# Optimization experiments

Hardware: AMD Instinct MI355X
Metric: run time of the kernel (lower is better)

The kernel has to match this reference:

```python
import jax, jax.numpy as jnp
import numpy as np
from jax import lax

E = 300   # word embedding dim (hard-coded embedding_size in DMCNN)
P = 5     # position-feature dim
H = 200   # conv out channels
S = 256   # max_seq_len
L = 34    # num_labels
VOCAB = 21128


def setup_inputs() -> dict:
    key = jax.random.key(0)
    ks = jax.random.split(key, 7)
    B = 8
    return {
        "inputs": jax.random.randint(ks[0], (B, S), 0, VOCAB, dtype=jnp.int64),
        "word_emb": jax.random.normal(ks[1], (VOCAB, E), dtype=jnp.float32) * 0.02,
        "pf_emb": jax.random.normal(ks[2], (S, P), dtype=jnp.float32) * 0.02,
        "conv_W": jax.random.normal(ks[3], (H, E + P, 3), dtype=jnp.float32) * 0.02,
        "conv_b": jax.random.normal(ks[4], (H,), dtype=jnp.float32) * 0.02,
        "fc_W": jax.random.normal(ks[5], (L, 3 * E + 2 * H), dtype=jnp.float32) * 0.02,
        "fc_b": jax.random.normal(ks[6], (L,), dtype=jnp.float32) * 0.02,
    }


def _conv1d(x_ncs, w_oik):
    # x: [N, C, S], w: [O, I, K], stride 1, padding 1 (kernel 3)
    return lax.conv_general_dilated(
        x_ncs, w_oik, window_strides=(1,), padding=[(1, 1)],
        dimension_numbers=("NCH", "OIH", "NCH"))


def reference(inputs, word_emb, pf_emb, conv_W, conv_b, fc_W, fc_b):
    B = inputs.shape[0]
    tok = word_emb[inputs]                       # [B, S, E]

    # Positions i = 1 .. S-2 (the original loop), fully vectorized.
    i_vals = jnp.arange(1, S - 1)                # [S-2]
    j = jnp.arange(S)
    pos_idx = jnp.abs(j[None, :] - i_vals[:, None])   # [S-2, S] == the loop's pos_index
    pf = pf_emb[pos_idx]                         # [S-2, S, P]

    # Conv is linear: split into token part (shared across i) + pf part (per i).
    W_tok, W_pf = conv_W[:, :E, :], conv_W[:, E:, :]
    conv_tok = _conv1d(tok.transpose(0, 2, 1), W_tok) + conv_b[None, :, None]  # [B, H, S]
    conv_pf = _conv1d(pf.transpose(0, 2, 1), W_pf)                             # [S-2, H, S] (batch-independent)

    out = jax.nn.relu(conv_tok[None] + conv_pf[:, None])   # [S-2, B, H, S]

    # Dynamic split max-pool at index i.
    left_mask = (j[None, :] < i_vals[:, None])[:, None, None, :]  # [S-2,1,1,S]
    neg_inf = jnp.array(-jnp.inf, dtype=out.dtype)
    max_left = jnp.where(left_mask, out, neg_inf).max(axis=-1)    # [S-2, B, H]
    max_right = jnp.where(left_mask, neg_inf, out).max(axis=-1)   # [S-2, B, H]
    pool = jnp.concatenate([max_left, max_right], axis=-1)        # [S-2, B, 2H]

    # Lexical-level features: window [i-1, i, i+1] flattened.
    llf = jnp.concatenate([tok[:, 0:S - 2], tok[:, 1:S - 1], tok[:, 2:S]], axis=-1)  # [B, S-2, 3E]

    feat = jnp.concatenate([pool.transpose(1, 0, 2), llf], axis=-1)  # [B, S-2, 2H+3E]
    logits_mid = jnp.einsum("bsf,lf->bsl", feat, fc_W) + fc_b        # [B, S-2, L]

    pad = jnp.zeros((B, 1, L), dtype=logits_mid.dtype).at[:, :, -1].set(1.0)
    return jnp.concatenate([pad, logits_mid, pad], axis=1)          # [B, S, L]
```

## Files before the change

kernel.cpp:

```cpp
#include <hip/hip_runtime.h>

#define E 300
#define P 5
#define H 200
#define S 256
#define L 34
#define B 8
#define NI 254

typedef __attribute__((ext_vector_type(8))) _Float16 half8;
typedef __attribute__((ext_vector_type(2))) _Float16 h2;
typedef __attribute__((ext_vector_type(4))) float f32x4;

#define TOKB_OFF   0
#define WR3_OFF    309632
#define FCWB_OFF   406144
#define G_OFF      438400
#define C0_OFF     489600
#define C255_OFF   515000
#define CT_OFF     540400
#define POOLF_OFF  745200

__device__ __forceinline__ unsigned short f2h(float f) {
    _Float16 h = (_Float16)f;
    unsigned short u; __builtin_memcpy(&u, &h, 2);
    return u;
}
__device__ __forceinline__ h2 u2h2(unsigned u) {
    h2 h; __builtin_memcpy(&h, &u, 4); return h;
}
__device__ __forceinline__ unsigned h2u(h2 h) {
    unsigned u; __builtin_memcpy(&u, &h, 4); return u;
}
__device__ __forceinline__ h2 hmax2(h2 a, h2 b) {
    return __builtin_elementwise_max(a, b);
}
__device__ __forceinline__ half8 load_h8(const unsigned short* p) {
    half8 r;
    ((ushort4*)&r)[0] = *(const ushort4*)p;
    ((ushort4*)&r)[1] = *(const ushort4*)(p + 4);
    return r;
}

#define GA_BLOCKS   605
#define WR3_BLOCKS  754
#define FCW_BLOCKS  252
#define PREP_BLOCKS 64
#define INIT_BLOCKS (GA_BLOCKS + WR3_BLOCKS + FCW_BLOCKS + PREP_BLOCKS)

__global__ __launch_bounds__(256) void k_init(const int* __restrict__ ids,
                                              const float* __restrict__ we,
                                              const float* __restrict__ convW,
                                              const float* __restrict__ fcW,
                                              const float* __restrict__ pf,
                                              unsigned short* __restrict__ tokb,
                                              unsigned short* __restrict__ Wr3,
                                              unsigned short* __restrict__ fcWb,
                                              unsigned short* __restrict__ g,
                                              unsigned short* __restrict__ c0,
                                              unsigned short* __restrict__ c255) {
    int bx = blockIdx.x;
    if (bx < GA_BLOCKS) {
        int idx = bx * 256 + threadIdx.x;
        const int total = B * 258 * 75;
        if (idx >= total) return;
        int row = idx / 75;
        int col = idx - row * 75;
        int b = row / 258;
        int r = row - b * 258;
        float4 v = make_float4(0.f, 0.f, 0.f, 0.f);
        if (r >= 1 && r <= 256) {
            int id = ids[b * S + (r - 1)];
            v = ((const float4*)we)[(size_t)id * 75 + col];
        }
        ushort4 o;
        o.x = f2h(v.x); o.y = f2h(v.y); o.z = f2h(v.z); o.w = f2h(v.w);
        *(ushort4*)(tokb + (size_t)row * 300 + col * 4) = o;
        return;
    }
    if (bx < GA_BLOCKS + WR3_BLOCKS) {
        int idx = (bx - GA_BLOCKS) * 256 + threadIdx.x;
        if (idx < 193024) {
            int hh = idx / 928, kk = idx - hh * 928;
            float v = 0.f;
            if (hh < H && kk < 900) {
                int r = kk / 300, e = kk - r * 300;
                v = convW[hh * 915 + e * 3 + r];
            }
            Wr3[idx] = f2h(v);
        }
        return;
    }
    if (bx < GA_BLOCKS + WR3_BLOCKS + FCW_BLOCKS) {
        int t = (bx - GA_BLOCKS - WR3_BLOCKS) * 256 + threadIdx.x;
        if (t < 64512) {
            int l = t / 1344, c = t - l * 1344;
            float v = 0.f;
            if (l < L) {
                if (c < 400) v = fcW[l * 1300 + c];
                else if (c >= 416 && c < 1316) v = fcW[l * 1300 + 400 + (c - 416)];
            }
            fcWb[t] = f2h(v);
        }
        return;
    }
    {
        __shared__ float cwg[200 * 15];
        int tid = threadIdx.x;
        if (tid < 200) {
            const float* src = convW + tid * 915 + 900;
#pragma unroll
            for (int i = 0; i < 15; i++) cwg[tid * 15 + i] = src[i];
        }
        __syncthreads();
        if (tid >= 200) return;
        int h = tid;
        int pb = bx - (GA_BLOCKS + WR3_BLOCKS + FCW_BLOCKS);
#pragma unroll 1
        for (int rl = 0; rl < 16; rl++) {
            int rg = pb * 16 + rl;
            if (rg >= 1020) break;
            float a = 0.f;
            if (rg < 512) {
                int d = rg - 256;
#pragma unroll
                for (int k = 0; k < 3; k++) {
                    int r = d + k - 1; r = (r < 0) ? -r : r; if (r > 255) r = 255;
#pragma unroll
                    for (int q = 0; q < P; q++)
                        a += cwg[h * 15 + q * 3 + k] * pf[r * P + q];
                }
                g[rg * H + h] = f2h(a);
            } else if (rg < 766) {
                int m = rg - 512, i = m + 1;
#pragma unroll
                for (int q = 0; q < P; q++) {
                    a += cwg[h * 15 + q * 3 + 1] * pf[i * P + q];
                    a += cwg[h * 15 + q * 3 + 2] * pf[(i - 1) * P + q];
                }
                c0[m * H + h] = f2h(a);
            } else {
                int m = rg - 766, i = m + 1;
#pragma unroll
                for (int q = 0; q < P; q++) {
                    a += cwg[h * 15 + q * 3 + 0] * pf[(254 - i) * P + q];
                    a += cwg[h * 15 + q * 3 + 1] * pf[(255 - i) * P + q];
                }
                c255[m * H + h] = f2h(a);
            }
        }
    }
}

__global__ __launch_bounds__(512) void k_conv(const unsigned short* __restrict__ tokb,
                                              const unsigned short* __restrict__ Wr3,
                                              const float* __restrict__ convB,
                                              unsigned short* __restrict__ ct) {
    __shared__ float4 cld[4 * 64];
    int n0 = blockIdx.x * 16;
    int mg = blockIdx.y;
    int tid = threadIdx.x;
    int wave = tid >> 6;
    int lane = tid & 63;
    int mt = wave & 3;
    int kh = wave >> 2;
    int quad = lane >> 4;
    int lr = lane & 15;
    int mtile = mg * 4 + mt;
    int b = mtile >> 4;
    int j0 = (mtile & 15) << 4;

    const unsigned short* pa = tokb + ((size_t)(b * 258 + j0 + lr) * 300 + quad * 8);
    const unsigned short* pb = Wr3 + ((size_t)(n0 + lr) * 928 + quad * 8);

    f32x4 acc0 = {0.f, 0.f, 0.f, 0.f};
    f32x4 acc1 = {0.f, 0.f, 0.f, 0.f};
    if (kh == 0) {
#pragma unroll
        for (int kk = 0; kk < 14; kk += 2) {
            half8 a0 = load_h8(pa + kk * 32);
            half8 b0 = load_h8(pb + kk * 32);
            acc0 = __builtin_amdgcn_mfma_f32_16x16x32_f16(a0, b0, acc0, 0, 0, 0);
            half8 a1 = load_h8(pa + kk * 32 + 32);
            half8 b1 = load_h8(pb + kk * 32 + 32);
            acc1 = __builtin_amdgcn_mfma_f32_16x16x32_f16(a1, b1, acc1, 0, 0, 0);
        }
    } else {
#pragma unroll
        for (int kk = 14; kk + 1 < 29; kk += 2) {
            half8 a0 = load_h8(pa + kk * 32);
            half8 b0 = load_h8(pb + kk * 32);
            acc0 = __builtin_amdgcn_mfma_f32_16x16x32_f16(a0, b0, acc0, 0, 0, 0);
            half8 a1 = load_h8(pa + kk * 32 + 32);
            half8 b1 = load_h8(pb + kk * 32 + 32);
            acc1 = __builtin_amdgcn_mfma_f32_16x16x32_f16(a1, b1, acc1, 0, 0, 0);
        }
        {
            half8 a0 = load_h8(pa + 28 * 32);
            half8 b0 = load_h8(pb + 28 * 32);
            acc0 = __builtin_amdgcn_mfma_f32_16x16x32_f16(a0, b0, acc0, 0, 0, 0);
        }
    }
    f32x4 accw = acc0 + acc1;
    if (kh == 1) {
        cld[mt * 64 + lane] = make_float4(accw[0], accw[1], accw[2], accw[3]);
    }
    __syncthreads();
    if (kh == 0) {
        float4 p = cld[mt * 64 + lane];
        int h = n0 + lr;
        if (h < H) {
            float bias = convB[h];
            ct[(size_t)(b * 256 + j0 + quad * 4 + 0) * 200 + h] = f2h(accw[0] + p.x + bias);
            ct[(size_t)(b * 256 + j0 + quad * 4 + 1) * 200 + h] = f2h(accw[1] + p.y + bias);
            ct[(size_t)(b * 256 + j0 + quad * 4 + 2) * 200 + h] = f2h(accw[2] + p.z + bias);
            ct[(size_t)(b * 256 + j0 + quad * 4 + 3) * 200 + h] = f2h(accw[3] + p.w + bias);
        }
    }
}

__global__ __launch_bounds__(512) void k_poolA(const unsigned short* __restrict__ ct,
                                               const unsigned short* __restrict__ g,
                                               const unsigned short* __restrict__ c0,
                                               const unsigned short* __restrict__ c255,
                                               unsigned short* __restrict__ poolf) {
    __shared__ uint2 lds2[8 * 4 * 2 * 50];
    int pg = blockIdx.x;
    int b  = blockIdx.y;
    int tid = threadIdx.x;
    int sub = tid >> 6;
    int lane = tid & 63;
    int p0 = pg * 4 + 1;

    if (lane < 50) {
        int h = lane << 2;
        const unsigned short* ctb = ct + (size_t)b * S * H + h;
        const unsigned short* gb  = g + h;

        h2 z = {(_Float16)0, (_Float16)0};
        h2 aL0a=z, aL0b=z, aL1a=z, aL1b=z, aL2a=z, aL2b=z, aL3a=z, aL3b=z;
        h2 aR0a=z, aR0b=z, aR1a=z, aR1b=z, aR2a=z, aR2b=z, aR3a=z, aR3b=z;

        if (sub == 0) {
            uint2 cu = *(const uint2*)ctb;
            h2 ca = u2h2(cu.x), cb = u2h2(cu.y);
            int m = pg * 4;
            if (m + 0 < NI) { uint2 t = *(const uint2*)(c0 + (m+0) * H + h);
                aL0a = hmax2(aL0a, ca + u2h2(t.x)); aL0b = hmax2(aL0b, cb + u2h2(t.y)); }
            if (m + 1 < NI) { uint2 t = *(const uint2*)(c0 + (m+1) * H + h);
                aL1a = hmax2(aL1a, ca + u2h2(t.x)); aL1b = hmax2(aL1b, cb + u2h2(t.y)); }
            if (m + 2 < NI) { uint2 t = *(const uint2*)(c0 + (m+2) * H + h);
                aL2a = hmax2(aL2a, ca + u2h2(t.x)); aL2b = hmax2(aL2b, cb + u2h2(t.y)); }
            if (m + 3 < NI) { uint2 t = *(const uint2*)(c0 + (m+3) * H + h);
                aL3a = hmax2(aL3a, ca + u2h2(t.x)); aL3b = hmax2(aL3b, cb + u2h2(t.y)); }
        }
        if (sub == 7) {
            uint2 cu = *(const uint2*)(ctb + (size_t)255 * H);
            h2 ca = u2h2(cu.x), cb = u2h2(cu.y);
            int m = pg * 4;
            if (m + 0 < NI) { uint2 t = *(const uint2*)(c255 + (m+0) * H + h);
                aR0a = hmax2(aR0a, ca + u2h2(t.x)); aR0b = hmax2(aR0b, cb + u2h2(t.y)); }
            if (m + 1 < NI) { uint2 t = *(const uint2*)(c255 + (m+1) * H + h);
                aR1a = hmax2(aR1a, ca + u2h2(t.x)); aR1b = hmax2(aR1b, cb + u2h2(t.y)); }
            if (m + 2 < NI) { uint2 t = *(const uint2*)(c255 + (m+2) * H + h);
                aR2a = hmax2(aR2a, ca + u2h2(t.x)); aR2b = hmax2(aR2b, cb + u2h2(t.y)); }
            if (m + 3 < NI) { uint2 t = *(const uint2*)(c255 + (m+3) * H + h);
                aR3a = hmax2(aR3a, ca + u2h2(t.x)); aR3b = hmax2(aR3b, cb + u2h2(t.y)); }
        }

        int js = (sub == 0) ? 1 : sub * 32;
        int je = (sub == 7) ? 254 : sub * 32 + 31;

        uint2 gu;
        gu = *(const uint2*)(gb + (size_t)(js - p0 + 256) * H); h2 gr0a = u2h2(gu.x), gr0b = u2h2(gu.y);
        gu = *(const uint2*)(gb + (size_t)(js - p0 + 255) * H); h2 gr1a = u2h2(gu.x), gr1b = u2h2(gu.y);
        gu = *(const uint2*)(gb + (size_t)(js - p0 + 254) * H); h2 gr2a = u2h2(gu.x), gr2b = u2h2(gu.y);
        gu = *(const uint2*)(gb + (size_t)(js - p0 + 253) * H); h2 gr3a = u2h2(gu.x), gr3b = u2h2(gu.y);

        int eL = (je + 1 < p0) ? (je + 1) : p0;
        int mS = (js > p0) ? js : p0;
        int eM = (je + 1 < p0 + 4) ? (je + 1) : (p0 + 4);
        int rS = (js > p0 + 4) ? js : (p0 + 4);

#pragma unroll 4
        for (int j = js; j < eL; ++j) {
            uint2 cu = *(const uint2*)(ctb + (size_t)j * H);
            h2 ca = u2h2(cu.x), cb = u2h2(cu.y);
            aL0a = hmax2(aL0a, ca + gr0a); aL0b = hmax2(aL0b, cb + gr0b);
            aL1a = hmax2(aL1a, ca + gr1a); aL1b = hmax2(aL1b, cb + gr1b);
            aL2a = hmax2(aL2a, ca + gr2a); aL2b = hmax2(aL2b, cb + gr2b);
            aL3a = hmax2(aL3a, ca + gr3a); aL3b = hmax2(aL3b, cb + gr3b);
            gr3a = gr2a; gr3b = gr2b; gr2a = gr1a; gr2b = gr1b; gr1a = gr0a; gr1b = gr0b;
            uint2 gn = *(const uint2*)(gb + (size_t)(j + 1 - p0 + 256) * H);
            gr0a = u2h2(gn.x); gr0b = u2h2(gn.y);
        }
        for (int j = mS; j < eM; ++j) {
            uint2 cu = *(const uint2*)(ctb + (size_t)j * H);
            h2 ca = u2h2(cu.x), cb = u2h2(cu.y);
            h2 v0a = ca + gr0a, v0b = cb + gr0b;
            h2 v1a = ca + gr1a, v1b = cb + gr1b;
            h2 v2a = ca + gr2a, v2b = cb + gr2b;
            h2 v3a = ca + gr3a, v3b = cb + gr3b;
            if (j < p0)     { aL0a = hmax2(aL0a, v0a); aL0b = hmax2(aL0b, v0b); }
            else            { aR0a = hmax2(aR0a, v0a); aR0b = hmax2(aR0b, v0b); }
            if (j < p0 + 1) { aL1a = hmax2(aL1a, v1a); aL1b = hmax2(aL1b, v1b); }
            else            { aR1a = hmax2(aR1a, v1a); aR1b = hmax2(aR1b, v1b); }
            if (j < p0 + 2) { aL2a = hmax2(aL2a, v2a); aL2b = hmax2(aL2b, v2b); }
            else            { aR2a = hmax2(aR2a, v2a); aR2b = hmax2(aR2b, v2b); }
            if (j < p0 + 3) { aL3a = hmax2(aL3a, v3a); aL3b = hmax2(aL3b, v3b); }
            else            { aR3a = hmax2(aR3a, v3a); aR3b = hmax2(aR3b, v3b); }
            gr3a = gr2a; gr3b = gr2b; gr2a = gr1a; gr2b = gr1b; gr1a = gr0a; gr1b = gr0b;
            uint2 gn = *(const uint2*)(gb + (size_t)(j + 1 - p0 + 256) * H);
            gr0a = u2h2(gn.x); gr0b = u2h2(gn.y);
        }
#pragma unroll 4
        for (int j = rS; j <= je; ++j) {
            uint2 cu = *(const uint2*)(ctb + (size_t)j * H);
            h2 ca = u2h2(cu.x), cb = u2h2(cu.y);
            aR0a = hmax2(aR0a, ca + gr0a); aR0b = hmax2(aR0b, cb + gr0b);
            aR1a = hmax2(aR1a, ca + gr1a); aR1b = hmax2(aR1b, cb + gr1b);
            aR2a = hmax2(aR2a, ca + gr2a); aR2b = hmax2(aR2b, cb + gr2b);
            aR3a = hmax2(aR3a, ca + gr3a); aR3b = hmax2(aR3b, cb + gr3b);
            gr3a = gr2a; gr3b = gr2b; gr2a = gr1a; gr2b = gr1b; gr1a = gr0a; gr1b = gr0b;
            uint2 gn = *(const uint2*)(gb + (size_t)(j + 1 - p0 + 256) * H);
            gr0a = u2h2(gn.x); gr0b = u2h2(gn.y);
        }

        uint2* lp = lds2 + (size_t)sub * 400 + lane;
        lp[0]   = make_uint2(h2u(aL0a), h2u(aL0b)); lp[50]  = make_uint2(h2u(aR0a), h2u(aR0b));
        lp[100] = make_uint2(h2u(aL1a), h2u(aL1b)); lp[150] = make_uint2(h2u(aR1a), h2u(aR1b));
        lp[200] = make_uint2(h2u(aL2a), h2u(aL2b)); lp[250] = make_uint2(h2u(aR2a), h2u(aR2b));
        lp[300] = make_uint2(h2u(aL3a), h2u(aL3b)); lp[350] = make_uint2(h2u(aR3a), h2u(aR3b));
    }
    __syncthreads();

    if (tid < 400) {
        int k = tid / 100;
        int r = tid - k * 100;
        int hf = r / 50;
        int ln = r - hf * 50;
        int slot = (k * 2 + hf) * 50 + ln;
        uint2 v = lds2[slot];
        h2 va = u2h2(v.x), vb = u2h2(v.y);
#pragma unroll
        for (int s2 = 1; s2 < 8; s2++) {
            uint2 w = lds2[s2 * 400 + slot];
            va = hmax2(va, u2h2(w.x));
            vb = hmax2(vb, u2h2(w.y));
        }
        int m = pg * 4 + k;
        if (m < NI)
            *(uint2*)(poolf + (size_t)(b * 256 + m + 1) * 416 + hf * 200 + ln * 4)
                = make_uint2(h2u(va), h2u(vb));
    } else if (tid < 464) {
        int t = tid - 400;
        int k = t >> 4, c = t & 15;
        int m = pg * 4 + k;
        if (m < NI) poolf[(size_t)(b * 256 + m + 1) * 416 + 400 + c] = 0;
    }
}

__global__ __launch_bounds__(512) void k_fc(const unsigned short* __restrict__ poolf,
                                            const unsigned short* __restrict__ tokb,
                                            const unsigned short* __restrict__ fcWb,
                                            const float* __restrict__ fcB,
                                            float* __restrict__ out) {
    __shared__ float4 cld[3 * 2 * 64];
    int n0 = blockIdx.x * 16;
    int mg = blockIdx.y;
    int tid = threadIdx.x;
    int wave = tid >> 6;
    int lane = tid & 63;
    int mt = wave & 1;
    int kp = wave >> 1;
    int quad = lane >> 4;
    int lr = lane & 15;
    int mtile = mg * 2 + mt;
    int b = mtile >> 4;
    int s0 = (mtile & 15) << 4;

    const unsigned short* pa0 = poolf + ((size_t)(b * 256 + s0 + lr) * 416 + quad * 8);
    const unsigned short* pb0 = fcWb + ((size_t)(n0 + lr) * 1344 + quad * 8);
    const unsigned short* pa1 = tokb + ((size_t)(b * 258 + s0 + lr) * 300 + quad * 8);
    const unsigned short* pb1 = fcWb + ((size_t)(n0 + lr) * 1344 + 416 + quad * 8);

    f32x4 acc0 = {0.f, 0.f, 0.f, 0.f};
    f32x4 acc1 = {0.f, 0.f, 0.f, 0.f};
    if (kp == 0) {
#pragma unroll
        for (int u = 0; u + 1 < 11; u += 2) {
            half8 a0 = load_h8(pa0 + u * 32);
            half8 b0 = load_h8(pb0 + u * 32);
            acc0 = __builtin_amdgcn_mfma_f32_16x16x32_f16(a0, b0, acc0, 0, 0, 0);
            half8 a1 = load_h8(pa0 + u * 32 + 32);
            half8 b1 = load_h8(pb0 + u * 32 + 32);
            acc1 = __builtin_amdgcn_mfma_f32_16x16x32_f16(a1, b1, acc1, 0, 0, 0);
        }
        {
            half8 a0 = load_h8(pa0 + 10 * 32);
            half8 b0 = load_h8(pb0 + 10 * 32);
            acc0 = __builtin_amdgcn_mfma_f32_16x16x32_f16(a0, b0, acc0, 0, 0, 0);
        }
    } else if (kp == 1) {
        {
            half8 a0 = load_h8(pa0 + 11 * 32);
            half8 b0 = load_h8(pb0 + 11 * 32);
            acc0 = __builtin_amdgcn_mfma_f32_16x16x32_f16(a0, b0, acc0, 0, 0, 0);
            half8 a1 = load_h8(pa0 + 12 * 32);
            half8 b1 = load_h8(pb0 + 12 * 32);
            acc1 = __builtin_amdgcn_mfma_f32_16x16x32_f16(a1, b1, acc1, 0, 0, 0);
        }
#pragma unroll
        for (int v = 0; v + 1 < 9; v += 2) {
            half8 a0 = load_h8(pa1 + v * 32);
            half8 b0 = load_h8(pb1 + v * 32);
            acc0 = __builtin_amdgcn_mfma_f32_16x16x32_f16(a0, b0, acc0, 0, 0, 0);
            half8 a1 = load_h8(pa1 + v * 32 + 32);
            half8 b1 = load_h8(pb1 + v * 32 + 32);
            acc1 = __builtin_amdgcn_mfma_f32_16x16x32_f16(a1, b1, acc1, 0, 0, 0);
        }
        {
            half8 a0 = load_h8(pa1 + 8 * 32);
            half8 b0 = load_h8(pb1 + 8 * 32);
            acc0 = __builtin_amdgcn_mfma_f32_16x16x32_f16(a0, b0, acc0, 0, 0, 0);
        }
    } else if (kp == 2) {
#pragma unroll
        for (int v = 9; v + 1 < 19; v += 2) {
            half8 a0 = load_h8(pa1 + v * 32);
            half8 b0 = load_h8(pb1 + v * 32);
            acc0 = __builtin_amdgcn_mfma_f32_16x16x32_f16(a0, b0, acc0, 0, 0, 0);
            half8 a1 = load_h8(pa1 + v * 32 + 32);
            half8 b1 = load_h8(pb1 + v * 32 + 32);
            acc1 = __builtin_amdgcn_mfma_f32_16x16x32_f16(a1, b1, acc1, 0, 0, 0);
        }
    } else {
#pragma unroll
        for (int v = 19; v + 1 < 29; v += 2) {
            half8 a0 = load_h8(pa1 + v * 32);
            half8 b0 = load_h8(pb1 + v * 32);
            acc0 = __builtin_amdgcn_mfma_f32_16x16x32_f16(a0, b0, acc0, 0, 0, 0);
            half8 a1 = load_h8(pa1 + v * 32 + 32);
            half8 b1 = load_h8(pb1 + v * 32 + 32);
            acc1 = __builtin_amdgcn_mfma_f32_16x16x32_f16(a1, b1, acc1, 0, 0, 0);
        }
    }
    f32x4 accw = acc0 + acc1;
    if (kp > 0) {
        cld[((kp - 1) * 2 + mt) * 64 + lane] = make_float4(accw[0], accw[1], accw[2], accw[3]);
    }
    __syncthreads();
    if (kp == 0) {
        float4 p1 = cld[(0 * 2 + mt) * 64 + lane];
        float4 p2 = cld[(1 * 2 + mt) * 64 + lane];
        float4 p3 = cld[(2 * 2 + mt) * 64 + lane];
        float r4[4] = {accw[0] + p1.x + p2.x + p3.x,
                       accw[1] + p1.y + p2.y + p3.y,
                       accw[2] + p1.z + p2.z + p3.z,
                       accw[3] + p1.w + p2.w + p3.w};
        int l = n0 + lr;
        if (l < L) {
            float bias = fcB[l];
#pragma unroll
            for (int r = 0; r < 4; r++) {
                int s = s0 + quad * 4 + r;
                float val;
                if (s == 0 || s == S - 1) val = (l == L - 1) ? 1.0f : 0.0f;
                else                      val = r4[r] + bias;
                out[(size_t)(b * 256 + s) * L + l] = val;
            }
        }
    }
}

extern "C" void kernel_launch(void* const* d_in, const int* in_sizes, int n_in,
                              void* d_out, int out_size, void* d_ws, size_t ws_size,
                              hipStream_t stream) {
    const int*   ids      = (const int*)d_in[0];
    const float* word_emb = (const float*)d_in[1];
    const float* pf_emb   = (const float*)d_in[2];
    const float* conv_W   = (const float*)d_in[3];
    const float* conv_b   = (const float*)d_in[4];
    const float* fc_W     = (const float*)d_in[5];
    const float* fc_b     = (const float*)d_in[6];
    float* out = (float*)d_out;
    float* ws  = (float*)d_ws;

    unsigned short* tokb  = (unsigned short*)(ws + TOKB_OFF);
    unsigned short* Wr3   = (unsigned short*)(ws + WR3_OFF);
    unsigned short* fcWb  = (unsigned short*)(ws + FCWB_OFF);
    unsigned short* g     = (unsigned short*)(ws + G_OFF);
    unsigned short* c0    = (unsigned short*)(ws + C0_OFF);
    unsigned short* c255  = (unsigned short*)(ws + C255_OFF);
    unsigned short* ct    = (unsigned short*)(ws + CT_OFF);
    unsigned short* poolf = (unsigned short*)(ws + POOLF_OFF);

    k_init<<<INIT_BLOCKS, 256, 0, stream>>>(ids, word_emb, conv_W, fc_W,
                                            pf_emb, tokb, Wr3, fcWb,
                                            g, c0, c255);
    k_conv<<<dim3(13, 32), 512, 0, stream>>>(tokb, Wr3, conv_b, ct);
    k_poolA<<<dim3(64, 8), 512, 0, stream>>>(ct, g, c0, c255, poolf);
    k_fc<<<dim3(3, 64), 512, 0, stream>>>(poolf, tokb, fcWb, fc_b, out);
}
```

Measured before the change: 114.5 us.

## Fuse conv, pool and fc kernels into one persistent kernel with grid barriers

Merges the three dependent kernels (conv GEMM, split max-pool, fc GEMM) into a single 512-block launch. A hierarchical atomic grid barrier in workspace memory separates the stages, and a memset clears it before each run. This removes two kernel launch boundaries and their drain and ramp gaps. In exchange it adds a memset launch and atomic spin-waits, and it relies on all 512 blocks being co-resident; the spin has a timeout break that could silently yield wrong results if they are not.

```diff
diff --git a/kernel.cpp b/kernel.cpp
--- a/kernel.cpp
+++ b/kernel.cpp
@@ -7,6 +7,8 @@
 #define L 34
 #define B 8
 #define NI 254
+#define NBLK 512
+#define NGRP 8
 
 typedef __attribute__((ext_vector_type(8))) _Float16 half8;
 typedef __attribute__((ext_vector_type(2))) _Float16 h2;
@@ -20,6 +22,7 @@
 #define C255_OFF   515000
 #define CT_OFF     540400
 #define POOLF_OFF  745200
+#define BAR_OFF    2000000
 
 __device__ __forceinline__ unsigned short f2h(float f) {
     _Float16 h = (_Float16)f;
@@ -47,6 +50,27 @@
 #define FCW_BLOCKS  252
 #define PREP_BLOCKS 64
 #define INIT_BLOCKS (GA_BLOCKS + WR3_BLOCKS + FCW_BLOCKS + PREP_BLOCKS)
+
+__device__ __forceinline__ void gbar(unsigned* bar, int phase) {
+    __syncthreads();
+    if (threadIdx.x == 0) {
+        unsigned* base = bar + phase * 1024;
+        unsigned* c1 = base + (blockIdx.x >> 6) * 16;
+        unsigned* c2 = base + 1008;
+        unsigned prev = __hip_atomic_fetch_add(c1, 1u, __ATOMIC_ACQ_REL,
+                                               __HIP_MEMORY_SCOPE_AGENT);
+        if (prev == 63)
+            __hip_atomic_fetch_add(c2, 1u, __ATOMIC_ACQ_REL,
+                                   __HIP_MEMORY_SCOPE_AGENT);
+        unsigned t = 0;
+        while (__hip_atomic_load(c2, __ATOMIC_ACQUIRE,
+                                 __HIP_MEMORY_SCOPE_AGENT) < NGRP) {
+            __builtin_amdgcn_s_sleep(2);
+            if (++t > (1u << 22)) break;
+        }
+    }
+    __syncthreads();
+}
 
 __global__ __launch_bounds__(256) void k_init(const int* __restrict__ ids,
                                               const float* __restrict__ we,
@@ -152,322 +176,328 @@
     }
 }
 
-__global__ __launch_bounds__(512) void k_conv(const unsigned short* __restrict__ tokb,
-                                              const unsigned short* __restrict__ Wr3,
-                                              const float* __restrict__ convB,
-                                              unsigned short* __restrict__ ct) {
-    __shared__ float4 cld[4 * 64];
-    int n0 = blockIdx.x * 16;
-    int mg = blockIdx.y;
-    int tid = threadIdx.x;
-    int wave = tid >> 6;
-    int lane = tid & 63;
-    int mt = wave & 3;
-    int kh = wave >> 2;
-    int quad = lane >> 4;
-    int lr = lane & 15;
-    int mtile = mg * 4 + mt;
-    int b = mtile >> 4;
-    int j0 = (mtile & 15) << 4;
-
-    const unsigned short* pa = tokb + ((size_t)(b * 258 + j0 + lr) * 300 + quad * 8);
-    const unsigned short* pb = Wr3 + ((size_t)(n0 + lr) * 928 + quad * 8);
-
-    f32x4 acc0 = {0.f, 0.f, 0.f, 0.f};
-    f32x4 acc1 = {0.f, 0.f, 0.f, 0.f};
-    if (kh == 0) {
-#pragma unroll
-        for (int kk = 0; kk < 14; kk += 2) {
-            half8 a0 = load_h8(pa + kk * 32);
-            half8 b0 = load_h8(pb + kk * 32);
-            acc0 = __builtin_amdgcn_mfma_f32_16x16x32_f16(a0, b0, acc0, 0, 0, 0);
-            half8 a1 = load_h8(pa + kk * 32 + 32);
-            half8 b1 = load_h8(pb + kk * 32 + 32);
-            acc1 = __builtin_amdgcn_mfma_f32_16x16x32_f16(a1, b1, acc1, 0, 0, 0);
-        }
-    } else {
-#pragma unroll
-        for (int kk = 14; kk + 1 < 29; kk += 2) {
-            half8 a0 = load_h8(pa + kk * 32);
-            half8 b0 = load_h8(pb + kk * 32);
-            acc0 = __builtin_amdgcn_mfma_f32_16x16x32_f16(a0, b0, acc0, 0, 0, 0);
-            half8 a1 = load_h8(pa + kk * 32 + 32);
-            half8 b1 = load_h8(pb + kk * 32 + 32);
-            acc1 = __builtin_amdgcn_mfma_f32_16x16x32_f16(a1, b1, acc1, 0, 0, 0);
-        }
-        {
-            half8 a0 = load_h8(pa + 28 * 32);
-            half8 b0 = load_h8(pb + 28 * 32);
-            acc0 = __builtin_amdgcn_mfma_f32_16x16x32_f16(a0, b0, acc0, 0, 0, 0);
-        }
-    }
-    f32x4 accw = acc0 + acc1;
-    if (kh == 1) {
-        cld[mt * 64 + lane] = make_float4(accw[0], accw[1], accw[2], accw[3]);
-    }
-    __syncthreads();
-    if (kh == 0) {
-        float4 p = cld[mt * 64 + lane];
-        int h = n0 + lr;
-        if (h < H) {
-            float bias = convB[h];
-            ct[(size_t)(b * 256 + j0 + quad * 4 + 0) * 200 + h] = f2h(accw[0] + p.x + bias);
-            ct[(size_t)(b * 256 + j0 + quad * 4 + 1) * 200 + h] = f2h(accw[1] + p.y + bias);
-            ct[(size_t)(b * 256 + j0 + quad * 4 + 2) * 200 + h] = f2h(accw[2] + p.z + bias);
-            ct[(size_t)(b * 256 + j0 + quad * 4 + 3) * 200 + h] = f2h(accw[3] + p.w + bias);
-        }
-    }
-}
-
-__global__ __launch_bounds__(512) void k_poolA(const unsigned short* __restrict__ ct,
-                                               const unsigned short* __restrict__ g,
-                                               const unsigned short* __restrict__ c0,
-                                               const unsigned short* __restrict__ c255,
-                                               unsigned short* __restrict__ poolf) {
-    __shared__ uint2 lds2[8 * 4 * 2 * 50];
-    int pg = blockIdx.x;
-    int b  = blockIdx.y;
-    int tid = threadIdx.x;
-    int sub = tid >> 6;
-    int lane = tid & 63;
-    int p0 = pg * 4 + 1;
-
-    if (lane < 50) {
-        int h = lane << 2;
-        const unsigned short* ctb = ct + (size_t)b * S * H + h;
-        const unsigned short* gb  = g + h;
-
-        h2 z = {(_Float16)0, (_Float16)0};
-        h2 aL0a=z, aL0b=z, aL1a=z, aL1b=z, aL2a=z, aL2b=z, aL3a=z, aL3b=z;
-        h2 aR0a=z, aR0b=z, aR1a=z, aR1b=z, aR2a=z, aR2b=z, aR3a=z, aR3b=z;
-
-        if (sub == 0) {
-            uint2 cu = *(const uint2*)ctb;
-            h2 ca = u2h2(cu.x), cb = u2h2(cu.y);
-            int m = pg * 4;
-            if (m + 0 < NI) { uint2 t = *(const uint2*)(c0 + (m+0) * H + h);
-                aL0a = hmax2(aL0a, ca + u2h2(t.x)); aL0b = hmax2(aL0b, cb + u2h2(t.y)); }
-            if (m + 1 < NI) { uint2 t = *(const uint2*)(c0 + (m+1) * H + h);
-                aL1a = hmax2(aL1a, ca + u2h2(t.x)); aL1b = hmax2(aL1b, cb + u2h2(t.y)); }
-            if (m + 2 < NI) { uint2 t = *(const uint2*)(c0 + (m+2) * H + h);
-                aL2a = hmax2(aL2a, ca + u2h2(t.x)); aL2b = hmax2(aL2b, cb + u2h2(t.y)); }
-            if (m + 3 < NI) { uint2 t = *(const uint2*)(c0 + (m+3) * H + h);
-                aL3a = hmax2(aL3a, ca + u2h2(t.x)); aL3b = hmax2(aL3b, cb + u2h2(t.y)); }
-        }
-        if (sub == 7) {
-            uint2 cu = *(const uint2*)(ctb + (size_t)255 * H);
-            h2 ca = u2h2(cu.x), cb = u2h2(cu.y);
-            int m = pg * 4;
-            if (m + 0 < NI) { uint2 t = *(const uint2*)(c255 + (m+0) * H + h);
-                aR0a = hmax2(aR0a, ca + u2h2(t.x)); aR0b = hmax2(aR0b, cb + u2h2(t.y)); }
-            if (m + 1 < NI) { uint2 t = *(const uint2*)(c255 + (m+1) * H + h);
-                aR1a = hmax2(aR1a, ca + u2h2(t.x)); aR1b = hmax2(aR1b, cb + u2h2(t.y)); }
-            if (m + 2 < NI) { uint2 t = *(const uint2*)(c255 + (m+2) * H + h);
-                aR2a = hmax2(aR2a, ca + u2h2(t.x)); aR2b = hmax2(aR2b, cb + u2h2(t.y)); }
-            if (m + 3 < NI) { uint2 t = *(const uint2*)(c255 + (m+3) * H + h);
-                aR3a = hmax2(aR3a, ca + u2h2(t.x)); aR3b = hmax2(aR3b, cb + u2h2(t.y)); }
-        }
-
-        int js = (sub == 0) ? 1 : sub * 32;
-        int je = (sub == 7) ? 254 : sub * 32 + 31;
-
-        uint2 gu;
-        gu = *(const uint2*)(gb + (size_t)(js - p0 + 256) * H); h2 gr0a = u2h2(gu.x), gr0b = u2h2(gu.y);
-        gu = *(const uint2*)(gb + (size_t)(js - p0 + 255) * H); h2 gr1a = u2h2(gu.x), gr1b = u2h2(gu.y);
-        gu = *(const uint2*)(gb + (size_t)(js - p0 + 254) * H); h2 gr2a = u2h2(gu.x), gr2b = u2h2(gu.y);
-        gu = *(const uint2*)(gb + (size_t)(js - p0 + 253) * H); h2 gr3a = u2h2(gu.x), gr3b = u2h2(gu.y);
-
-        int eL = (je + 1 < p0) ? (je + 1) : p0;
-        int mS = (js > p0) ? js : p0;
-        int eM = (je + 1 < p0 + 4) ? (je + 1) : (p0 + 4);
-        int rS = (js > p0 + 4) ? js : (p0 + 4);
+__global__ __launch_bounds__(512, 4) void k_bcd(
+        const unsigned short* __restrict__ tokb,
+        const unsigned short* __restrict__ Wr3,
+        const float* __restrict__ convB,
+        const unsigned short* __restrict__ g,
+        const unsigned short* __restrict__ c0,
+        const unsigned short* __restrict__ c255,
+        const unsigned short* __restrict__ fcWb,
+        const float* __restrict__ fcB,
+        unsigned short* __restrict__ ct,
+        unsigned short* __restrict__ poolf,
+        float* __restrict__ out,
+        unsigned* bar) {
+    __shared__ __align__(16) unsigned char smem[25600];
+    float4* cld = (float4*)smem;
+    uint2*  lds2 = (uint2*)smem;
+
+    const int bid = blockIdx.x;
+    const int tid = threadIdx.x;
+
+    if (bid < 416) {
+        int n0 = (bid % 13) * 16;
+        int mg = bid / 13;
+        int wave = tid >> 6;
+        int lane = tid & 63;
+        int mt = wave & 3;
+        int kh = wave >> 2;
+        int quad = lane >> 4;
+        int lr = lane & 15;
+        int mtile = mg * 4 + mt;
+        int b = mtile >> 4;
+        int j0 = (mtile & 15) << 4;
+
+        const unsigned short* pa = tokb + ((size_t)(b * 258 + j0 + lr) * 300 + quad * 8);
+        const unsigned short* pb = Wr3 + ((size_t)(n0 + lr) * 928 + quad * 8);
+
+        f32x4 acc0 = {0.f, 0.f, 0.f, 0.f};
+        f32x4 acc1 = {0.f, 0.f, 0.f, 0.f};
+        if (kh == 0) {
+#pragma unroll
+            for (int kk = 0; kk < 14; kk += 2) {
+                half8 a0 = load_h8(pa + kk * 32);
+                half8 b0 = load_h8(pb + kk * 32);
+                acc0 = __builtin_amdgcn_mfma_f32_16x16x32_f16(a0, b0, acc0, 0, 0, 0);
+                half8 a1 = load_h8(pa + kk * 32 + 32);
+                half8 b1 = load_h8(pb + kk * 32 + 32);
+                acc1 = __builtin_amdgcn_mfma_f32_16x16x32_f16(a1, b1, acc1, 0, 0, 0);
+            }
+        } else {
+#pragma unroll
+            for (int kk = 14; kk + 1 < 29; kk += 2) {
+                half8 a0 = load_h8(pa + kk * 32);
+                half8 b0 = load_h8(pb + kk * 32);
+                acc0 = __builtin_amdgcn_mfma_f32_16x16x32_f16(a0, b0, acc0, 0, 0, 0);
+                half8 a1 = load_h8(pa + kk * 32 + 32);
+                half8 b1 = load_h8(pb + kk * 32 + 32);
+                acc1 = __builtin_amdgcn_mfma_f32_16x16x32_f16(a1, b1, acc1, 0, 0, 0);
+            }
+            {
+                half8 a0 = load_h8(pa + 28 * 32);
+                half8 b0 = load_h8(pb + 28 * 32);
+                acc0 = __builtin_amdgcn_mfma_f32_16x16x32_f16(a0, b0, acc0, 0, 0, 0);
+            }
+        }
+        f32x4 accw = acc0 + acc1;
+        if (kh == 1) {
+            cld[mt * 64 + lane] = make_float4(accw[0], accw[1], accw[2], accw[3]);
+        }
+        __syncthreads();
+        if (kh == 0) {
+            float4 p = cld[mt * 64 + lane];
+            int h = n0 + lr;
+            if (h < H) {
+                float bias = convB[h];
+                ct[(size_t)(b * 256 + j0 + quad * 4 + 0) * 200 + h] = f2h(accw[0] + p.x + bias);
+                ct[(size_t)(b * 256 + j0 + quad * 4 + 1) * 200 + h] = f2h(accw[1] + p.y + bias);
+                ct[(size_t)(b * 256 + j0 + quad * 4 + 2) * 200 + h] = f2h(accw[2] + p.z + bias);
+                ct[(size_t)(b * 256 + j0 + quad * 4 + 3) * 200 + h] = f2h(accw[3] + p.w + bias);
+            }
+        }
+    }
+    gbar(bar, 0);
+
+    {
+        int pg = bid & 63;
+        int b  = bid >> 6;
+        int sub = tid >> 6;
+        int lane = tid & 63;
+        int p0 = pg * 4 + 1;
+
+        if (lane < 50) {
+            int h = lane << 2;
+            const unsigned short* ctb = ct + (size_t)b * S * H + h;
+            const unsigned short* gb  = g + h;
+
+            h2 z = {(_Float16)0, (_Float16)0};
+            h2 aL0a=z, aL0b=z, aL1a=z, aL1b=z, aL2a=z, aL2b=z, aL3a=z, aL3b=z;
+            h2 aR0a=z, aR0b=z, aR1a=z, aR1b=z, aR2a=z, aR2b=z, aR3a=z, aR3b=z;
+
+            if (sub == 0) {
+                uint2 cu = *(const uint2*)ctb;
+                h2 ca = u2h2(cu.x), cb = u2h2(cu.y);
+                int m = pg * 4;
+                if (m + 0 < NI) { uint2 t = *(const uint2*)(c0 + (m+0) * H + h);
+                    aL0a = hmax2(aL0a, ca + u2h2(t.x)); aL0b = hmax2(aL0b, cb + u2h2(t.y)); }
+                if (m + 1 < NI) { uint2 t = *(const uint2*)(c0 + (m+1) * H + h);
+                    aL1a = hmax2(aL1a, ca + u2h2(t.x)); aL1b = hmax2(aL1b, cb + u2h2(t.y)); }
+                if (m + 2 < NI) { uint2 t = *(const uint2*)(c0 + (m+2) * H + h);
+                    aL2a = hmax2(aL2a, ca + u2h2(t.x)); aL2b = hmax2(aL2b, cb + u2h2(t.y)); }
+                if (m + 3 < NI) { uint2 t = *(const uint2*)(c0 + (m+3) * H + h);
+                    aL3a = hmax2(aL3a, ca + u2h2(t.x)); aL3b = hmax2(aL3b, cb + u2h2(t.y)); }
+            }
+            if (sub == 7) {
+                uint2 cu = *(const uint2*)(ctb + (size_t)255 * H);
+                h2 ca = u2h2(cu.x), cb = u2h2(cu.y);
+                int m = pg * 4;
+                if (m + 0 < NI) { uint2 t = *(const uint2*)(c255 + (m+0) * H + h);
+                    aR0a = hmax2(aR0a, ca + u2h2(t.x)); aR0b = hmax2(aR0b, cb + u2h2(t.y)); }
+                if (m + 1 < NI) { uint2 t = *(const uint2*)(c255 + (m+1) * H + h);
+                    aR1a = hmax2(aR1a, ca + u2h2(t.x)); aR1b = hmax2(aR1b, cb + u2h2(t.y)); }
+                if (m + 2 < NI) { uint2 t = *(const uint2*)(c255 + (m+2) * H + h);
+                    aR2a = hmax2(aR2a, ca + u2h2(t.x)); aR2b = hmax2(aR2b, cb + u2h2(t.y)); }
+                if (m + 3 < NI) { uint2 t = *(const uint2*)(c255 + (m+3) * H + h);
+                    aR3a = hmax2(aR3a, ca + u2h2(t.x)); aR3b = hmax2(aR3b, cb + u2h2(t.y)); }
+            }
+
+            int js = (sub == 0) ? 1 : sub * 32;
+            int je = (sub == 7) ? 254 : sub * 32 + 31;
+
+            uint2 gu;
+            gu = *(const uint2*)(gb + (size_t)(js - p0 + 256) * H); h2 gr0a = u2h2(gu.x), gr0b = u2h2(gu.y);
+            gu = *(const uint2*)(gb + (size_t)(js - p0 + 255) * H); h2 gr1a = u2h2(gu.x), gr1b = u2h2(gu.y);
+            gu = *(const uint2*)(gb + (size_t)(js - p0 + 254) * H); h2 gr2a = u2h2(gu.x), gr2b = u2h2(gu.y);
+            gu = *(const uint2*)(gb + (size_t)(js - p0 + 253) * H); h2 gr3a = u2h2(gu.x), gr3b = u2h2(gu.y);
+
+            int eL = (je + 1 < p0) ? (je + 1) : p0;
+            int mS = (js > p0) ? js : p0;
+            int eM = (je + 1 < p0 + 4) ? (je + 1) : (p0 + 4);
+            int rS = (js > p0 + 4) ? js : (p0 + 4);
 
 #pragma unroll 4
-        for (int j = js; j < eL; ++j) {
-            uint2 cu = *(const uint2*)(ctb + (size_t)j * H);
-            h2 ca = u2h2(cu.x), cb = u2h2(cu.y);
-            aL0a = hmax2(aL0a, ca + gr0a); aL0b = hmax2(aL0b, cb + gr0b);
-            aL1a = hmax2(aL1a, ca + gr1a); aL1b = hmax2(aL1b, cb + gr1b);
-            aL2a = hmax2(aL2a, ca + gr2a); aL2b = hmax2(aL2b, cb + gr2b);
-            aL3a = hmax2(aL3a, ca + gr3a); aL3b = hmax2(aL3b, cb + gr3b);
-            gr3a = gr2a; gr3b = gr2b; gr2a = gr1a; gr2b = gr1b; gr1a = gr0a; gr1b = gr0b;
-            uint2 gn = *(const uint2*)(gb + (size_t)(j + 1 - p0 + 256) * H);
-            gr0a = u2h2(gn.x); gr0b = u2h2(gn.y);
-        }
-        for (int j = mS; j < eM; ++j) {
-            uint2 cu = *(const uint2*)(ctb + (size_t)j * H);
-            h2 ca = u2h2(cu.x), cb = u2h2(cu.y);
-            h2 v0a = ca + gr0a, v0b = cb + gr0b;
-            h2 v1a = ca + gr1a, v1b = cb + gr1b;
-            h2 v2a = ca + gr2a, v2b = cb + gr2b;
-            h2 v3a = ca + gr3a, v3b = cb + gr3b;
-            if (j < p0)     { aL0a = hmax2(aL0a, v0a); aL0b = hmax2(aL0b, v0b); }
-            else            { aR0a = hmax2(aR0a, v0a); aR0b = hmax2(aR0b, v0b); }
-            if (j < p0 + 1) { aL1a = hmax2(aL1a, v1a); aL1b = hmax2(aL1b, v1b); }
-            else            { aR1a = hmax2(aR1a, v1a); aR1b = hmax2(aR1b, v1b); }
-            if (j < p0 + 2) { aL2a = hmax2(aL2a, v2a); aL2b = hmax2(aL2b, v2b); }
-            else            { aR2a = hmax2(aR2a, v2a); aR2b = hmax2(aR2b, v2b); }
-            if (j < p0 + 3) { aL3a = hmax2(aL3a, v3a); aL3b = hmax2(aL3b, v3b); }
-            else            { aR3a = hmax2(aR3a, v3a); aR3b = hmax2(aR3b, v3b); }
-            gr3a = gr2a; gr3b = gr2b; gr2a = gr1a; gr2b = gr1b; gr1a = gr0a; gr1b = gr0b;
-            uint2 gn = *(const uint2*)(gb + (size_t)(j + 1 - p0 + 256) * H);
-            gr0a = u2h2(gn.x); gr0b = u2h2(gn.y);
-        }
+            for (int j = js; j < eL; ++j) {
+                uint2 cu = *(const uint2*)(ctb + (size_t)j * H);
+                h2 ca = u2h2(cu.x), cb = u2h2(cu.y);
+                aL0a = hmax2(aL0a, ca + gr0a); aL0b = hmax2(aL0b, cb + gr0b);
+                aL1a = hmax2(aL1a, ca + gr1a); aL1b = hmax2(aL1b, cb + gr1b);
+                aL2a = hmax2(aL2a, ca + gr2a); aL2b = hmax2(aL2b, cb + gr2b);
+                aL3a = hmax2(aL3a, ca + gr3a); aL3b = hmax2(aL3b, cb + gr3b);
+                gr3a = gr2a; gr3b = gr2b; gr2a = gr1a; gr2b = gr1b; gr1a = gr0a; gr1b = gr0b;
+                uint2 gn = *(const uint2*)(gb + (size_t)(j + 1 - p0 + 256) * H);
+                gr0a = u2h2(gn.x); gr0b = u2h2(gn.y);
+            }
+            for (int j = mS; j < eM; ++j) {
+                uint2 cu = *(const uint2*)(ctb + (size_t)j * H);
+                h2 ca = u2h2(cu.x), cb = u2h2(cu.y);
+                h2 v0a = ca + gr0a, v0b = cb + gr0b;
+                h2 v1a = ca + gr1a, v1b = cb + gr1b;
+                h2 v2a = ca + gr2a, v2b = cb + gr2b;
+                h2 v3a = ca + gr3a, v3b = cb + gr3b;
+                if (j < p0)     { aL0a = hmax2(aL0a, v0a); aL0b = hmax2(aL0b, v0b); }
+                else            { aR0a = hmax2(aR0a, v0a); aR0b = hmax2(aR0b, v0b); }
+                if (j < p0 + 1) { aL1a = hmax2(aL1a, v1a); aL1b = hmax2(aL1b, v1b); }
+                else            { aR1a = hmax2(aR1a, v1a); aR1b = hmax2(aR1b, v1b); }
+                if (j < p0 + 2) { aL2a = hmax2(aL2a, v2a); aL2b = hmax2(aL2b, v2b); }
+                else            { aR2a = hmax2(aR2a, v2a); aR2b = hmax2(aR2b, v2b); }
+                if (j < p0 + 3) { aL3a = hmax2(aL3a, v3a); aL3b = hmax2(aL3b, v3b); }
+                else            { aR3a = hmax2(aR3a, v3a); aR3b = hmax2(aR3b, v3b); }
+                gr3a = gr2a; gr3b = gr2b; gr2a = gr1a; gr2b = gr1b; gr1a = gr0a; gr1b = gr0b;
+                uint2 gn = *(const uint2*)(gb + (size_t)(j + 1 - p0 + 256) * H);
+                gr0a = u2h2(gn.x); gr0b = u2h2(gn.y);
+            }
 #pragma unroll 4
-        for (int j = rS; j <= je; ++j) {
-            uint2 cu = *(const uint2*)(ctb + (size_t)j * H);
-            h2 ca = u2h2(cu.x), cb = u2h2(cu.y);
-            aR0a = hmax2(aR0a, ca + gr0a); aR0b = hmax2(aR0b, cb + gr0b);
-            aR1a = hmax2(aR1a, ca + gr1a); aR1b = hmax2(aR1b, cb + gr1b);
-            aR2a = hmax2(aR2a, ca + gr2a); aR2b = hmax2(aR2b, cb + gr2b);
-            aR3a = hmax2(aR3a, ca + gr3a); aR3b = hmax2(aR3b, cb + gr3b);
-            gr3a = gr2a; gr3b = gr2b; gr2a = gr1a; gr2b = gr1b; gr1a = gr0a; gr1b = gr0b;
-            uint2 gn = *(const uint2*)(gb + (size_t)(j + 1 - p0 + 256) * H);
-            gr0a = u2h2(gn.x); gr0b = u2h2(gn.y);
-        }
-
-        uint2* lp = lds2 + (size_t)sub * 400 + lane;
-        lp[0]   = make_uint2(h2u(aL0a), h2u(aL0b)); lp[50]  = make_uint2(h2u(aR0a), h2u(aR0b));
-        lp[100] = make_uint2(h2u(aL1a), h2u(aL1b)); lp[150] = make_uint2(h2u(aR1a), h2u(aR1b));
-        lp[200] = make_uint2(h2u(aL2a), h2u(aL2b)); lp[250] = make_uint2(h2u(aR2a), h2u(aR2b));
-        lp[300] = make_uint2(h2u(aL3a), h2u(aL3b)); lp[350] = make_uint2(h2u(aR3a), h2u(aR3b));
-    }
-    __syncthreads();
-
-    if (tid < 400) {
-        int k = tid / 100;
-        int r = tid - k * 100;
-        int hf = r / 50;
-        int ln = r - hf * 50;
-        int slot = (k * 2 + hf) * 50 + ln;
-        uint2 v = lds2[slot];
-        h2 va = u2h2(v.x), vb = u2h2(v.y);
-#pragma unroll
-        for (int s2 = 1; s2 < 8; s2++) {
-            uint2 w = lds2[s2 * 400 + slot];
-            va = hmax2(va, u2h2(w.x));
-            vb = hmax2(vb, u2h2(w.y));
-        }
-        int m = pg * 4 + k;
-        if (m < NI)
-            *(uint2*)(poolf + (size_t)(b * 256 + m + 1) * 416 + hf * 200 + ln * 4)
-                = make_uint2(h2u(va), h2u(vb));
-    } else if (tid < 464) {
-        int t = tid - 400;
-        int k = t >> 4, c = t & 15;
-        int m = pg * 4 + k;
-        if (m < NI) poolf[(size_t)(b * 256 + m + 1) * 416 + 400 + c] = 0;
-    }
-}
-
-__global__ __launch_bounds__(512) void k_fc(const unsigned short* __restrict__ poolf,
-                                            const unsigned short* __restrict__ tokb,
-                                            const unsigned short* __restrict__ fcWb,
-                                            const float* __restrict__ fcB,
-                                            float* __restrict__ out) {
-    __shared__ float4 cld[3 * 2 * 64];
-    int n0 = blockIdx.x * 16;
-    int mg = blockIdx.y;
-    int tid = threadIdx.x;
-    int wave = tid >> 6;
-    int lane = tid & 63;
-    int mt = wave & 1;
-    int kp = wave >> 1;
-    int quad = lane >> 4;
-    int lr = lane & 15;
-    int mtile = mg * 2 + mt;
-    int b = mtile >> 4;
-    int s0 = (mtile & 15) << 4;
-
-    const unsigned short* pa0 = poolf + ((size_t)(b * 256 + s0 + lr) * 416 + quad * 8);
-    const unsigned short* pb0 = fcWb + ((size_t)(n0 + lr) * 1344 + quad * 8);
-    const unsigned short* pa1 = tokb + ((size_t)(b * 258 + s0 + lr) * 300 + quad * 8);
-    const unsigned short* pb1 = fcWb + ((size_t)(n0 + lr) * 1344 + 416 + quad * 8);
-
-    f32x4 acc0 = {0.f, 0.f, 0.f, 0.f};
-    f32x4 acc1 = {0.f, 0.f, 0.f, 0.f};
-    if (kp == 0) {
-#pragma unroll
-        for (int u = 0; u + 1 < 11; u += 2) {
-            half8 a0 = load_h8(pa0 + u * 32);
-            half8 b0 = load_h8(pb0 + u * 32);
-            acc0 = __builtin_amdgcn_mfma_f32_16x16x32_f16(a0, b0, acc0, 0, 0, 0);
-            half8 a1 = load_h8(pa0 + u * 32 + 32);
-            half8 b1 = load_h8(pb0 + u * 32 + 32);
-            acc1 = __builtin_amdgcn_mfma_f32_16x16x32_f16(a1, b1, acc1, 0, 0, 0);
-        }
-        {
-            half8 a0 = load_h8(pa0 + 10 * 32);
-            half8 b0 = load_h8(pb0 + 10 * 32);
-            acc0 = __builtin_amdgcn_mfma_f32_16x16x32_f16(a0, b0, acc0, 0, 0, 0);
-        }
-    } else if (kp == 1) {
-        {
-            half8 a0 = load_h8(pa0 + 11 * 32);
-            half8 b0 = load_h8(pb0 + 11 * 32);
-            acc0 = __builtin_amdgcn_mfma_f32_16x16x32_f16(a0, b0, acc0, 0, 0, 0);
-            half8 a1 = load_h8(pa0 + 12 * 32);
-            half8 b1 = load_h8(pb0 + 12 * 32);
-            acc1 = __builtin_amdgcn_mfma_f32_16x16x32_f16(a1, b1, acc1, 0, 0, 0);
-        }
-#pragma unroll
-        for (int v = 0; v + 1 < 9; v += 2) {
-            half8 a0 = load_h8(pa1 + v * 32);
-            half8 b0 = load_h8(pb1 + v * 32);
-            acc0 = __builtin_amdgcn_mfma_f32_16x16x32_f16(a0, b0, acc0, 0, 0, 0);
-            half8 a1 = load_h8(pa1 + v * 32 + 32);
-            half8 b1 = load_h8(pb1 + v * 32 + 32);
-            acc1 = __builtin_amdgcn_mfma_f32_16x16x32_f16(a1, b1, acc1, 0, 0, 0);
-        }
-        {
-            half8 a0 = load_h8(pa1 + 8 * 32);
-            half8 b0 = load_h8(pb1 + 8 * 32);
-            acc0 = __builtin_amdgcn_mfma_f32_16x16x32_f16(a0, b0, acc0, 0, 0, 0);
-        }
-    } else if (kp == 2) {
-#pragma unroll
-        for (int v = 9; v + 1 < 19; v += 2) {
-            half8 a0 = load_h8(pa1 + v * 32);
-            half8 b0 = load_h8(pb1 + v * 32);
-            acc0 = __builtin_amdgcn_mfma_f32_16x16x32_f16(a0, b0, acc0, 0, 0, 0);
-            half8 a1 = load_h8(pa1 + v * 32 + 32);
-            half8 b1 = load_h8(pb1 + v * 32 + 32);
-            acc1 = __builtin_amdgcn_mfma_f32_16x16x32_f16(a1, b1, acc1, 0, 0, 0);
-        }
-    } else {
-#pragma unroll
-        for (int v = 19; v + 1 < 29; v += 2) {
-            half8 a0 = load_h8(pa1 + v * 32);
-            half8 b0 = load_h8(pb1 + v * 32);
-            acc0 = __builtin_amdgcn_mfma_f32_16x16x32_f16(a0, b0, acc0, 0, 0, 0);
-            half8 a1 = load_h8(pa1 + v * 32 + 32);
-            half8 b1 = load_h8(pb1 + v * 32 + 32);
-            acc1 = __builtin_amdgcn_mfma_f32_16x16x32_f16(a1, b1, acc1, 0, 0, 0);
-        }
-    }
-    f32x4 accw = acc0 + acc1;
-    if (kp > 0) {
-        cld[((kp - 1) * 2 + mt) * 64 + lane] = make_float4(accw[0], accw[1], accw[2], accw[3]);
-    }
-    __syncthreads();
-    if (kp == 0) {
-        float4 p1 = cld[(0 * 2 + mt) * 64 + lane];
-        float4 p2 = cld[(1 * 2 + mt) * 64 + lane];
-        float4 p3 = cld[(2 * 2 + mt) * 64 + lane];
-        float r4[4] = {accw[0] + p1.x + p2.x + p3.x,
-                       accw[1] + p1.y + p2.y + p3.y,
-                       accw[2] + p1.z + p2.z + p3.z,
-                       accw[3] + p1.w + p2.w + p3.w};
-        int l = n0 + lr;
-        if (l < L) {
-            float bias = fcB[l];
-#pragma unroll
-            for (int r = 0; r < 4; r++) {
-                int s = s0 + quad * 4 + r;
-                float val;
-                if (s == 0 || s == S - 1) val = (l == L - 1) ? 1.0f : 0.0f;
-                else                      val = r4[r] + bias;
-                out[(size_t)(b * 256 + s) * L + l] = val;
+            for (int j = rS; j <= je; ++j) {
+                uint2 cu = *(const uint2*)(ctb + (size_t)j * H);
+                h2 ca = u2h2(cu.x), cb = u2h2(cu.y);
+                aR0a = hmax2(aR0a, ca + gr0a); aR0b = hmax2(aR0b, cb + gr0b);
+                aR1a = hmax2(aR1a, ca + gr1a); aR1b = hmax2(aR1b, cb + gr1b);
+                aR2a = hmax2(aR2a, ca + gr2a); aR2b = hmax2(aR2b, cb + gr2b);
+                aR3a = hmax2(aR3a, ca + gr3a); aR3b = hmax2(aR3b, cb + gr3b);
+                gr3a = gr2a; gr3b = gr2b; gr2a = gr1a; gr2b = gr1b; gr1a = gr0a; gr1b = gr0b;
+                uint2 gn = *(const uint2*)(gb + (size_t)(j + 1 - p0 + 256) * H);
+                gr0a = u2h2(gn.x); gr0b = u2h2(gn.y);
+            }
+
+            uint2* lp = lds2 + (size_t)sub * 400 + lane;
+            lp[0]   = make_uint2(h2u(aL0a), h2u(aL0b)); lp[50]  = make_uint2(h2u(aR0a), h2u(aR0b));
+            lp[100] = make_uint2(h2u(aL1a), h2u(aL1b)); lp[150] = make_uint2(h2u(aR1a), h2u(aR1b));
+            lp[200] = make_uint2(h2u(aL2a), h2u(aL2b)); lp[250] = make_uint2(h2u(aR2a), h2u(aR2b));
+            lp[300] = make_uint2(h2u(aL3a), h2u(aL3b)); lp[350] = make_uint2(h2u(aR3a), h2u(aR3b));
+        }
+        __syncthreads();
+
+        if (tid < 400) {
+            int k = tid / 100;
+            int r = tid - k * 100;
+            int hf = r / 50;
+            int ln = r - hf * 50;
+            int slot = (k * 2 + hf) * 50 + ln;
+            uint2 v = lds2[slot];
+            h2 va = u2h2(v.x), vb = u2h2(v.y);
+#pragma unroll
+            for (int s2 = 1; s2 < 8; s2++) {
+                uint2 w = lds2[s2 * 400 + slot];
+                va = hmax2(va, u2h2(w.x));
+                vb = hmax2(vb, u2h2(w.y));
+            }
+            int m = pg * 4 + k;
+            if (m < NI)
+                *(uint2*)(poolf + (size_t)(b * 256 + m + 1) * 416 + hf * 200 + ln * 4)
+                    = make_uint2(h2u(va), h2u(vb));
+        } else if (tid < 464) {
+            int t = tid - 400;
+            int k = t >> 4, c = t & 15;
+            int m = pg * 4 + k;
+            if (m < NI) poolf[(size_t)(b * 256 + m + 1) * 416 + 400 + c] = 0;
+        }
+    }
+    gbar(bar, 1);
+
+    if (bid < 192) {
+        int n0 = (bid % 3) * 16;
+        int mg = bid / 3;
+        int wave = tid >> 6;
+        int lane = tid & 63;
+        int mt = wave & 1;
+        int kp = wave >> 1;
+        int quad = lane >> 4;
+        int lr = lane & 15;
+        int mtile = mg * 2 + mt;
+        int b = mtile >> 4;
+        int s0 = (mtile & 15) << 4;
+
+        const unsigned short* pa0 = poolf + ((size_t)(b * 256 + s0 + lr) * 416 + quad * 8);
+        const unsigned short* pb0 = fcWb + ((size_t)(n0 + lr) * 1344 + quad * 8);
+        const unsigned short* pa1 = tokb + ((size_t)(b * 258 + s0 + lr) * 300 + quad * 8);
+        const unsigned short* pb1 = fcWb + ((size_t)(n0 + lr) * 1344 + 416 + quad * 8);
+
+        f32x4 acc0 = {0.f, 0.f, 0.f, 0.f};
+        f32x4 acc1 = {0.f, 0.f, 0.f, 0.f};
+        if (kp == 0) {
+#pragma unroll
+            for (int u = 0; u + 1 < 11; u += 2) {
+                half8 a0 = load_h8(pa0 + u * 32);
+                half8 b0 = load_h8(pb0 + u * 32);
+                acc0 = __builtin_amdgcn_mfma_f32_16x16x32_f16(a0, b0, acc0, 0, 0, 0);
+                half8 a1 = load_h8(pa0 + u * 32 + 32);
+                half8 b1 = load_h8(pb0 + u * 32 + 32);
+                acc1 = __builtin_amdgcn_mfma_f32_16x16x32_f16(a1, b1, acc1, 0, 0, 0);
+            }
+            {
+                half8 a0 = load_h8(pa0 + 10 * 32);
+                half8 b0 = load_h8(pb0 + 10 * 32);
+                acc0 = __builtin_amdgcn_mfma_f32_16x16x32_f16(a0, b0, acc0, 0, 0, 0);
+            }
+        } else if (kp == 1) {
+            {
+                half8 a0 = load_h8(pa0 + 11 * 32);
+                half8 b0 = load_h8(pb0 + 11 * 32);
+                acc0 = __builtin_amdgcn_mfma_f32_16x16x32_f16(a0, b0, acc0, 0, 0, 0);
+                half8 a1 = load_h8(pa0 + 12 * 32);
+                half8 b1 = load_h8(pb0 + 12 * 32);
+                acc1 = __builtin_amdgcn_mfma_f32_16x16x32_f16(a1, b1, acc1, 0, 0, 0);
+            }
+#pragma unroll
+            for (int v = 0; v + 1 < 9; v += 2) {
+                half8 a0 = load_h8(pa1 + v * 32);
+                half8 b0 = load_h8(pb1 + v * 32);
+                acc0 = __builtin_amdgcn_mfma_f32_16x16x32_f16(a0, b0, acc0, 0, 0, 0);
+                half8 a1 = load_h8(pa1 + v * 32 + 32);
+                half8 b1 = load_h8(pb1 + v * 32 + 32);
+                acc1 = __builtin_amdgcn_mfma_f32_16x16x32_f16(a1, b1, acc1, 0, 0, 0);
+            }
+            {
+                half8 a0 = load_h8(pa1 + 8 * 32);
+                half8 b0 = load_h8(pb1 + 8 * 32);
+                acc0 = __builtin_amdgcn_mfma_f32_16x16x32_f16(a0, b0, acc0, 0, 0, 0);
+            }
+        } else if (kp == 2) {
+#pragma unroll
+            for (int v = 9; v + 1 < 19; v += 2) {
+                half8 a0 = load_h8(pa1 + v * 32);
+                half8 b0 = load_h8(pb1 + v * 32);
+                acc0 = __builtin_amdgcn_mfma_f32_16x16x32_f16(a0, b0, acc0, 0, 0, 0);
+                half8 a1 = load_h8(pa1 + v * 32 + 32);
+                half8 b1 = load_h8(pb1 + v * 32 + 32);
+                acc1 = __builtin_amdgcn_mfma_f32_16x16x32_f16(a1, b1, acc1, 0, 0, 0);
+            }
+        } else {
+#pragma unroll
+            for (int v = 19; v + 1 < 29; v += 2) {
+                half8 a0 = load_h8(pa1 + v * 32);
+                half8 b0 = load_h8(pb1 + v * 32);
+                acc0 = __builtin_amdgcn_mfma_f32_16x16x32_f16(a0, b0, acc0, 0, 0, 0);
+                half8 a1 = load_h8(pa1 + v * 32 + 32);
+                half8 b1 = load_h8(pb1 + v * 32 + 32);
+                acc1 = __builtin_amdgcn_mfma_f32_16x16x32_f16(a1, b1, acc1, 0, 0, 0);
+            }
+        }
+        f32x4 accw = acc0 + acc1;
+        if (kp > 0) {
+            cld[((kp - 1) * 2 + mt) * 64 + lane] = make_float4(accw[0], accw[1], accw[2], accw[3]);
+        }
+        __syncthreads();
+        if (kp == 0) {
+            float4 p1 = cld[(0 * 2 + mt) * 64 + lane];
+            float4 p2 = cld[(1 * 2 + mt) * 64 + lane];
+            float4 p3 = cld[(2 * 2 + mt) * 64 + lane];
+            float r4[4] = {accw[0] + p1.x + p2.x + p3.x,
+                           accw[1] + p1.y + p2.y + p3.y,
+                           accw[2] + p1.z + p2.z + p3.z,
+                           accw[3] + p1.w + p2.w + p3.w};
+            int l = n0 + lr;
+            if (l < L) {
+                float bias = fcB[l];
+#pragma unroll
+                for (int r = 0; r < 4; r++) {
+                    int s = s0 + quad * 4 + r;
+                    float val;
+                    if (s == 0 || s == S - 1) val = (l == L - 1) ? 1.0f : 0.0f;
+                    else                      val = r4[r] + bias;
+                    out[(size_t)(b * 256 + s) * L + l] = val;
+                }
             }
         }
     }
@@ -494,11 +524,12 @@
     unsigned short* c255  = (unsigned short*)(ws + C255_OFF);
     unsigned short* ct    = (unsigned short*)(ws + CT_OFF);
     unsigned short* poolf = (unsigned short*)(ws + POOLF_OFF);
-
+    unsigned*       bar   = (unsigned*)(ws + BAR_OFF);
+
+    hipMemsetAsync(bar, 0, 2 * 4096, stream);
     k_init<<<INIT_BLOCKS, 256, 0, stream>>>(ids, word_emb, conv_W, fc_W,
                                             pf_emb, tokb, Wr3, fcWb,
                                             g, c0, c255);
-    k_conv<<<dim3(13, 32), 512, 0, stream>>>(tokb, Wr3, conv_b, ct);
-    k_poolA<<<dim3(64, 8), 512, 0, stream>>>(ct, g, c0, c255, poolf);
-    k_fc<<<dim3(3, 64), 512, 0, stream>>>(poolf, tokb, fcWb, fc_b, out);
-}
+    k_bcd<<<NBLK, 512, 0, stream>>>(tokb, Wr3, conv_b, g, c0, c255,
+                                    fcWb, fc_b, ct, poolf, out, bar);
+}
```

Result: slower. 199.1 us (+73.9%).
